# Performance work log

Measured on AMD Instinct MI355X. Metric: run time of the kernel, lower is better.

## Reference

```python
import jax, jax.numpy as jnp
import numpy as np

KH, KW, PAD, G = 3, 3, 1, 4  # kernel, padding, deformable groups


def _bilinear_gather(xg, py, px):
    """xg: [B,G,C,Hin,Win]; py,px: [B,G,K,H,W] sample coords.
    Returns [B,G,C,K,H,W] with zero padding outside the image (mmcv semantics)."""
    B, Gd, C, Hin, Win = xg.shape
    y0 = jnp.floor(py)
    x0 = jnp.floor(px)
    wy1 = py - y0
    wx1 = px - x0
    wy0 = 1.0 - wy1
    wx0 = 1.0 - wx1
    xf = xg.reshape(B, Gd, C, Hin * Win)

    def gather(yi, xi):
        valid = (yi >= 0) & (yi < Hin) & (xi >= 0) & (xi < Win)
        yc = jnp.clip(yi, 0, Hin - 1).astype(jnp.int32)
        xc = jnp.clip(xi, 0, Win - 1).astype(jnp.int32)
        lin = (yc * Win + xc).reshape(B, Gd, 1, -1)  # [B,G,1,K*H*W]
        v = jnp.take_along_axis(xf, lin, axis=3).reshape(B, Gd, C, *yi.shape[2:])
        return v * valid[:, :, None].astype(xg.dtype)

    return (gather(y0, x0) * (wy0 * wx0)[:, :, None]
            + gather(y0, x0 + 1) * (wy0 * wx1)[:, :, None]
            + gather(y0 + 1, x0) * (wy1 * wx0)[:, :, None]
            + gather(y0 + 1, x0 + 1) * (wy1 * wx1)[:, :, None])


def setup_inputs() -> dict:
    key = jax.random.key(0)
    k1, k2, k3, k4 = jax.random.split(key, 4)
    B, Cin, Cout, H, W = 8, 256, 256, 64, 64
    x = jax.random.normal(k1, (B, Cin, H, W), dtype=jnp.float32)
    shape = jax.random.normal(k2, (B, 4, H, W), dtype=jnp.float32)
    # conv_offset: 1x1 conv, 4 -> G*2*KH*KW = 72 channels, no bias
    w_offset = jax.random.normal(k3, (G * 2 * KH * KW, 4), dtype=jnp.float32) * 0.1
    # conv_adaption: deform conv weight, no bias
    w_deform = jax.random.normal(k4, (Cout, Cin, KH, KW), dtype=jnp.float32) * 0.01
    return {"x": x, "shape": shape, "w_offset": w_offset, "w_deform": w_deform}


def reference(x, shape, w_offset, w_deform):
    B, Cin, H, W = x.shape
    Cout = w_deform.shape[0]
    K = KH * KW
    # 1x1 offset-predicting conv on detached shape
    shape = jax.lax.stop_gradient(shape)
    offset = jnp.einsum('oc,bchw->bohw', w_offset, shape)  # [B, G*2*K, H, W]
    off = offset.reshape(B, G, K, 2, H, W)  # mmcv layout: (dy, dx) per tap
    dy, dx = off[:, :, :, 0], off[:, :, :, 1]  # [B,G,K,H,W]
    # base sampling grid for each kernel tap
    ky, kx = jnp.meshgrid(jnp.arange(KH), jnp.arange(KW), indexing='ij')
    ky = ky.reshape(-1)
    kx = kx.reshape(-1)
    base_y = (ky - PAD)[:, None, None] + jnp.arange(H)[None, :, None]  # [K,H,1]
    base_x = (kx - PAD)[:, None, None] + jnp.arange(W)[None, None, :]  # [K,1,W]
    py = base_y[None, None].astype(x.dtype) + dy  # [B,G,K,H,W]
    px = base_x[None, None].astype(x.dtype) + dx
    xg = x.reshape(B, G, Cin // G, H, W)
    sampled = _bilinear_gather(xg, py, px)  # [B,G,Cpg,K,H,W]
    wr = w_deform.reshape(Cout, G, Cin // G, K)
    out = jnp.einsum('ogck,bgckhw->bohw', wr, sampled)
    return jax.nn.relu(out)
```

## Files before the change

kernel.cpp:

```cpp
#include <hip/hip_runtime.h>
#include <hip/hip_bf16.h>


#define Bn   8
#define CIN  256
#define COUT 256
#define Hn   64
#define Wn   64
#define Gn   4
#define Kn   9
#define CPG  64
#define GK   36

typedef __bf16 bf16x8 __attribute__((ext_vector_type(8)));
typedef float  f32x4  __attribute__((ext_vector_type(4)));

#define SWPAD 1156
__global__ void fa_prep(const float* __restrict__ x, const float* __restrict__ w,
                        __bf16* __restrict__ xt, __bf16* __restrict__ wfrag) {
    const int bid = blockIdx.x, t = threadIdx.x;
    __shared__ __bf16 sw[16 * SWPAD];
    if (bid < 4096) {
        const int c8q = bid & 7, hwt = (bid >> 3) & 63, b = bid >> 9;
        const int hw = hwt * 64 + (t & 63);
        const int c8 = c8q * 4 + (t >> 6);
        const float* xp = x + ((size_t)(b * CIN + c8 * 8) << 12) + hw;
        bf16x8 v;
#pragma unroll
        for (int j = 0; j < 8; j++) v[j] = (__bf16)xp[(size_t)j << 12];
        *(bf16x8*)&xt[(((size_t)b << 12) + hw) * 256 + c8 * 8] = v;
    } else {
        const int mt = (bid - 4096) >> 1, gh = (bid - 4096) & 1;
        const int o0 = mt * 16, g0 = gh * 2;
        const int r = t >> 4, tr = t & 15;
        const float* wp = w + (size_t)(o0 + r) * (CIN * Kn) + g0 * (CPG * Kn);
#pragma unroll
        for (int it = 0; it < 18; it++) {
            int off = it * 64 + tr * 4;
            float4 v = *(const float4*)(wp + off);
            __bf16* d = &sw[r * SWPAD + off];
            d[0] = (__bf16)v.x; d[1] = (__bf16)v.y;
            d[2] = (__bf16)v.z; d[3] = (__bf16)v.w;
        }
        __syncthreads();
#pragma unroll
        for (int it = 0; it < 9; it++) {
            int chunk = it * 256 + t;
            int lane = chunk & 63, ks = (chunk >> 6) & 1, gkl = chunk >> 7;
            int gl = gkl / Kn, k = gkl - gl * Kn;
            int gk = g0 * Kn + gkl;
            int ol = lane & 15;
            int cbase = ks * 32 + (lane >> 4) * 8;
            bf16x8 v;
#pragma unroll
            for (int j = 0; j < 8; j++)
                v[j] = sw[ol * SWPAD + (gl * CPG + cbase + j) * Kn + k];
            *(bf16x8*)&wfrag[(((size_t)gk * 16 + mt) * 2 + ks) * 512 + lane * 8] = v;
        }
    }
}

__global__ __launch_bounds__(256, 2)
void fa_main(const __bf16* __restrict__ xt, const float* __restrict__ shp,
             const float* __restrict__ w_off, const __bf16* __restrict__ wfrag,
             float* __restrict__ out) {
    const int blk = blockIdx.x;
    const int bp = blk >> 7, h = (blk >> 1) & 63, wh = blk & 1;
    const int w0 = wh * 32;
    const int t = threadIdx.x;
    const int wid = t >> 6, lane = t & 63;
    const int col = lane & 15, quad = lane >> 4;
    const int cg = t & 7, nl0 = t >> 3;

    __shared__ int   s_iyx[GK * 64];
    __shared__ float s_fy[GK * 64];
    __shared__ float s_fx[GK * 64];
    __shared__ __align__(16) __bf16 sB[2][64 * 64];

    for (int i = t; i < GK * 64; i += 256) {
        int gk = i >> 6, n = i & 63;
        int bb = n >> 5, w = w0 + (n & 31);
        int b = bp * 2 + bb;
        int g = gk / Kn, k = gk - g * Kn;
        int ky = k / 3, kx = k - ky * 3;
        int oy = (g * Kn + k) * 2;
        float dy = 0.f, dx = 0.f;
#pragma unroll
        for (int c = 0; c < 4; c++) {
            float sv = shp[((b * 4 + c) * Hn + h) * Wn + w];
            dy = fmaf(w_off[(oy    ) * 4 + c], sv, dy);
            dx = fmaf(w_off[(oy + 1) * 4 + c], sv, dx);
        }
        float py = (float)(h + ky - 1) + dy;
        float px = (float)(w + kx - 1) + dx;
        float y0 = floorf(py), x0 = floorf(px);
        s_fy[i] = py - y0;
        s_fx[i] = px - x0;
        s_iyx[i] = (((int)y0 & 0xffff) << 16) | ((int)x0 & 0xffff);
    }

    bf16x8 c4[2][4];
    float  w4[2][4];

    auto issue = [&](int gk) {
#pragma unroll
        for (int s = 0; s < 2; s++) {
            int n = nl0 + s * 32;
            int b = bp * 2 + (n >> 5);
            int m = gk * 64 + n;
            int g = gk / Kn;
            int pk = s_iyx[m];
            int iy = pk >> 16, ix = (pk << 16) >> 16;
            float fy = s_fy[m], fx = s_fx[m];
            bool y0v = (unsigned)iy       < (unsigned)Hn;
            bool y1v = (unsigned)(iy + 1) < (unsigned)Hn;
            bool x0v = (unsigned)ix       < (unsigned)Wn;
            bool x1v = (unsigned)(ix + 1) < (unsigned)Wn;
            int yc0 = min(max(iy, 0), Hn - 1), yc1 = min(max(iy + 1, 0), Hn - 1);
            int xc0 = min(max(ix, 0), Wn - 1), xc1 = min(max(ix + 1, 0), Wn - 1);
            const __bf16* base = xt + (((size_t)b << 12)) * 256 + g * CPG + cg * 8;
            c4[s][0] = *(const bf16x8*)(base + ((size_t)(yc0 * 64 + xc0)) * 256);
            c4[s][1] = *(const bf16x8*)(base + ((size_t)(yc0 * 64 + xc1)) * 256);
            c4[s][2] = *(const bf16x8*)(base + ((size_t)(yc1 * 64 + xc0)) * 256);
            c4[s][3] = *(const bf16x8*)(base + ((size_t)(yc1 * 64 + xc1)) * 256);
            float wy1 = fy, wy0 = 1.f - fy, wx1 = fx, wx0 = 1.f - fx;
            w4[s][0] = (y0v && x0v) ? wy0 * wx0 : 0.f;
            w4[s][1] = (y0v && x1v) ? wy0 * wx1 : 0.f;
            w4[s][2] = (y1v && x0v) ? wy1 * wx0 : 0.f;
            w4[s][3] = (y1v && x1v) ? wy1 * wx1 : 0.f;
        }
    };
    auto commit = [&](int buf) {
#pragma unroll
        for (int s = 0; s < 2; s++) {
            int n = nl0 + s * 32;
            bf16x8 r;
#pragma unroll
            for (int j = 0; j < 8; j++) {
                float v = w4[s][0] * (float)c4[s][0][j] + w4[s][1] * (float)c4[s][1][j]
                        + w4[s][2] * (float)c4[s][2][j] + w4[s][3] * (float)c4[s][3][j];
                r[j] = (__bf16)v;
            }
            *(bf16x8*)&sB[buf][(n * 8 + (cg ^ (n & 7))) * 8] = r;
        }
    };
    auto loadA = [&](int gk, bf16x8 af[2][4]) {
        const __bf16* wbase = wfrag + (((size_t)gk * 16 + wid * 4) * 2) * 512;
#pragma unroll
        for (int ks = 0; ks < 2; ks++)
#pragma unroll
            for (int mt = 0; mt < 4; mt++)
                af[ks][mt] = *(const bf16x8*)(wbase + ((size_t)(mt * 2 + ks) * 64 + lane) * 8);
    };

    f32x4 acc[4][4];
#pragma unroll
    for (int mt = 0; mt < 4; mt++)
#pragma unroll
        for (int nt = 0; nt < 4; nt++) acc[mt][nt] = (f32x4){0.f, 0.f, 0.f, 0.f};

    auto domfma = [&](bf16x8 af[2][4], int buf) {
#pragma unroll
        for (int ks = 0; ks < 2; ks++) {
            bf16x8 bfv[4];
#pragma unroll
            for (int nt = 0; nt < 4; nt++) {
                int n = nt * 16 + col;
                int cq8 = ks * 4 + quad;
                bfv[nt] = *(const bf16x8*)&sB[buf][(n * 8 + (cq8 ^ (n & 7))) * 8];
            }
#pragma unroll
            for (int mt = 0; mt < 4; mt++)
#pragma unroll
                for (int nt = 0; nt < 4; nt++)
                    acc[mt][nt] = __builtin_amdgcn_mfma_f32_16x16x32_bf16(
                        af[ks][mt], bfv[nt], acc[mt][nt], 0, 0, 0);
        }
    };

    bf16x8 afA[2][4], afB[2][4];

    __syncthreads();

    loadA(0, afA);
    issue(0);
    commit(0);
    issue(1);
    __syncthreads();

    for (int gk = 0; gk < GK; gk += 2) {
        loadA(gk + 1, afB);
        commit(1);
        if (gk + 2 < GK) issue(gk + 2);
        domfma(afA, 0);
        __syncthreads();
        if (gk + 2 < GK) loadA(gk + 2, afA);
        if (gk + 2 < GK) commit(0);
        if (gk + 3 < GK) issue(gk + 3);
        domfma(afB, 1);
        __syncthreads();
    }

#pragma unroll
    for (int mt = 0; mt < 4; mt++)
#pragma unroll
        for (int r = 0; r < 4; r++) {
            int o = wid * 64 + mt * 16 + quad * 4 + r;
#pragma unroll
            for (int nt = 0; nt < 4; nt++) {
                int n = nt * 16 + col;
                int b = bp * 2 + (n >> 5);
                int w = w0 + (n & 31);
                out[(((size_t)(b * COUT + o)) << 12) + h * Wn + w] =
                    fmaxf(acc[mt][nt][r], 0.f);
            }
        }
}

extern "C" void kernel_launch(void* const* d_in, const int* in_sizes, int n_in,
                              void* d_out, int out_size, void* d_ws, size_t ws_size,
                              hipStream_t stream) {
    const float* x     = (const float*)d_in[0];
    const float* shp   = (const float*)d_in[1];
    const float* w_off = (const float*)d_in[2];
    const float* w_def = (const float*)d_in[3];
    float* out = (float*)d_out;
    __bf16* wfrag = (__bf16*)d_ws;
    __bf16* xt    = (__bf16*)((char*)d_ws + (2u << 20));

    fa_prep<<<4096 + 32, 256, 0, stream>>>(x, w_def, xt, wfrag);
    fa_main<<<512, 256, 0, stream>>>(xt, shp, w_off, wfrag, out);
}
```

Before: 154.3 us.

## Use 512-thread blocks with eight waves splitting output channels in main kernel

```diff
diff --git a/kernel.cpp b/kernel.cpp
--- a/kernel.cpp
+++ b/kernel.cpp
@@ -60,7 +60,7 @@
     }
 }
 
-__global__ __launch_bounds__(256, 2)
+__global__ __launch_bounds__(512, 4)
 void fa_main(const __bf16* __restrict__ xt, const float* __restrict__ shp,
              const float* __restrict__ w_off, const __bf16* __restrict__ wfrag,
              float* __restrict__ out) {
@@ -70,14 +70,14 @@
     const int t = threadIdx.x;
     const int wid = t >> 6, lane = t & 63;
     const int col = lane & 15, quad = lane >> 4;
-    const int cg = t & 7, nl0 = t >> 3;
+    const int cg = t & 7, nl = (t >> 3) & 63;
 
     __shared__ int   s_iyx[GK * 64];
     __shared__ float s_fy[GK * 64];
     __shared__ float s_fx[GK * 64];
     __shared__ __align__(16) __bf16 sB[2][64 * 64];
 
-    for (int i = t; i < GK * 64; i += 256) {
+    for (int i = t; i < GK * 64; i += 512) {
         int gk = i >> 6, n = i & 63;
         int bb = n >> 5, w = w0 + (n & 31);
         int b = bp * 2 + bb;
@@ -99,67 +99,68 @@
         s_iyx[i] = (((int)y0 & 0xffff) << 16) | ((int)x0 & 0xffff);
     }
 
-    bf16x8 c4[2][4];
-    float  w4[2][4];
+    bf16x8 c4[4];
+    float  w4[4];
 
     auto issue = [&](int gk) {
-#pragma unroll
-        for (int s = 0; s < 2; s++) {
-            int n = nl0 + s * 32;
-            int b = bp * 2 + (n >> 5);
-            int m = gk * 64 + n;
-            int g = gk / Kn;
-            int pk = s_iyx[m];
-            int iy = pk >> 16, ix = (pk << 16) >> 16;
-            float fy = s_fy[m], fx = s_fx[m];
-            bool y0v = (unsigned)iy       < (unsigned)Hn;
-            bool y1v = (unsigned)(iy + 1) < (unsigned)Hn;
-            bool x0v = (unsigned)ix       < (unsigned)Wn;
-            bool x1v = (unsigned)(ix + 1) < (unsigned)Wn;
-            int yc0 = min(max(iy, 0), Hn - 1), yc1 = min(max(iy + 1, 0), Hn - 1);
-            int xc0 = min(max(ix, 0), Wn - 1), xc1 = min(max(ix + 1, 0), Wn - 1);
-            const __bf16* base = xt + (((size_t)b << 12)) * 256 + g * CPG + cg * 8;
-            c4[s][0] = *(const bf16x8*)(base + ((size_t)(yc0 * 64 + xc0)) * 256);
-            c4[s][1] = *(const bf16x8*)(base + ((size_t)(yc0 * 64 + xc1)) * 256);
-            c4[s][2] = *(const bf16x8*)(base + ((size_t)(yc1 * 64 + xc0)) * 256);
-            c4[s][3] = *(const bf16x8*)(base + ((size_t)(yc1 * 64 + xc1)) * 256);
-            float wy1 = fy, wy0 = 1.f - fy, wx1 = fx, wx0 = 1.f - fx;
-            w4[s][0] = (y0v && x0v) ? wy0 * wx0 : 0.f;
-            w4[s][1] = (y0v && x1v) ? wy0 * wx1 : 0.f;
-            w4[s][2] = (y1v && x0v) ? wy1 * wx0 : 0.f;
-            w4[s][3] = (y1v && x1v) ? wy1 * wx1 : 0.f;
-        }
+        int b = bp * 2 + (nl >> 5);
+        int m = gk * 64 + nl;
+        int g = gk / Kn;
+        int pk = s_iyx[m];
+        int iy = pk >> 16, ix = (pk << 16) >> 16;
+        float fy = s_fy[m], fx = s_fx[m];
+        bool y0v = (unsigned)iy       < (unsigned)Hn;
+        bool y1v = (unsigned)(iy + 1) < (unsigned)Hn;
+        bool x0v = (unsigned)ix       < (unsigned)Wn;
+        bool x1v = (unsigned)(ix + 1) < (unsigned)Wn;
+        int yc0 = min(max(iy, 0), Hn - 1), yc1 = min(max(iy + 1, 0), Hn - 1);
+        int xc0 = min(max(ix, 0), Wn - 1), xc1 = min(max(ix + 1, 0), Wn - 1);
+        const __bf16* base = xt + (((size_t)b << 12)) * 256 + g * CPG + cg * 8;
+        c4[0] = *(const bf16x8*)(base + ((size_t)(yc0 * 64 + xc0)) * 256);
+        c4[1] = *(const bf16x8*)(base + ((size_t)(yc0 * 64 + xc1)) * 256);
+        c4[2] = *(const bf16x8*)(base + ((size_t)(yc1 * 64 + xc0)) * 256);
+        c4[3] = *(const bf16x8*)(base + ((size_t)(yc1 * 64 + xc1)) * 256);
+        float wy1 = fy, wy0 = 1.f - fy, wx1 = fx, wx0 = 1.f - fx;
+        w4[0] = (y0v && x0v) ? wy0 * wx0 : 0.f;
+        w4[1] = (y0v && x1v) ? wy0 * wx1 : 0.f;
+        w4[2] = (y1v && x0v) ? wy1 * wx0 : 0.f;
+        w4[3] = (y1v && x1v) ? wy1 * wx1 : 0.f;
     };
     auto commit = [&](int buf) {
-#pragma unroll
-        for (int s = 0; s < 2; s++) {
-            int n = nl0 + s * 32;
-            bf16x8 r;
-#pragma unroll
-            for (int j = 0; j < 8; j++) {
-                float v = w4[s][0] * (float)c4[s][0][j] + w4[s][1] * (float)c4[s][1][j]
-                        + w4[s][2] * (float)c4[s][2][j] + w4[s][3] * (float)c4[s][3][j];
-                r[j] = (__bf16)v;
-            }
-            *(bf16x8*)&sB[buf][(n * 8 + (cg ^ (n & 7))) * 8] = r;
-        }
+        bf16x8 r;
+#pragma unroll
+        for (int j = 0; j < 8; j++) {
+            float v = w4[0] * (float)c4[0][j] + w4[1] * (float)c4[1][j]
+                    + w4[2] * (float)c4[2][j] + w4[3] * (float)c4[3][j];
+            r[j] = (__bf16)v;
+        }
+        *(bf16x8*)&sB[buf][(nl * 8 + (cg ^ (nl & 7))) * 8] = r;
     };
-    auto loadA = [&](int gk, bf16x8 af[2][4]) {
-        const __bf16* wbase = wfrag + (((size_t)gk * 16 + wid * 4) * 2) * 512;
+
+    f32x4 acc[2][4];
+#pragma unroll
+    for (int mt = 0; mt < 2; mt++)
+#pragma unroll
+        for (int nt = 0; nt < 4; nt++) acc[mt][nt] = (f32x4){0.f, 0.f, 0.f, 0.f};
+
+    __syncthreads();
+
+    issue(0);
+    commit(0);
+    issue(1);
+    __syncthreads();
+
+    for (int gk = 0; gk < GK; gk++) {
+        const int buf = gk & 1;
+        const __bf16* wbase = wfrag + (((size_t)gk * 16 + wid * 2) * 2) * 512;
+        bf16x8 af[2][2];
 #pragma unroll
         for (int ks = 0; ks < 2; ks++)
 #pragma unroll
-            for (int mt = 0; mt < 4; mt++)
+            for (int mt = 0; mt < 2; mt++)
                 af[ks][mt] = *(const bf16x8*)(wbase + ((size_t)(mt * 2 + ks) * 64 + lane) * 8);
-    };
-
-    f32x4 acc[4][4];
-#pragma unroll
-    for (int mt = 0; mt < 4; mt++)
-#pragma unroll
-        for (int nt = 0; nt < 4; nt++) acc[mt][nt] = (f32x4){0.f, 0.f, 0.f, 0.f};
-
-    auto domfma = [&](bf16x8 af[2][4], int buf) {
+        if (gk + 1 < GK) commit(buf ^ 1);
+        if (gk + 2 < GK) issue(gk + 2);
 #pragma unroll
         for (int ks = 0; ks < 2; ks++) {
             bf16x8 bfv[4];
@@ -170,42 +171,20 @@
                 bfv[nt] = *(const bf16x8*)&sB[buf][(n * 8 + (cq8 ^ (n & 7))) * 8];
             }
 #pragma unroll
-            for (int mt = 0; mt < 4; mt++)
+            for (int mt = 0; mt < 2; mt++)
 #pragma unroll
                 for (int nt = 0; nt < 4; nt++)
                     acc[mt][nt] = __builtin_amdgcn_mfma_f32_16x16x32_bf16(
                         af[ks][mt], bfv[nt], acc[mt][nt], 0, 0, 0);
         }
-    };
-
-    bf16x8 afA[2][4], afB[2][4];
-
-    __syncthreads();
-
-    loadA(0, afA);
-    issue(0);
-    commit(0);
-    issue(1);
-    __syncthreads();
-
-    for (int gk = 0; gk < GK; gk += 2) {
-        loadA(gk + 1, afB);
-        commit(1);
-        if (gk + 2 < GK) issue(gk + 2);
-        domfma(afA, 0);
-        __syncthreads();
-        if (gk + 2 < GK) loadA(gk + 2, afA);
-        if (gk + 2 < GK) commit(0);
-        if (gk + 3 < GK) issue(gk + 3);
-        domfma(afB, 1);
         __syncthreads();
     }
 
 #pragma unroll
-    for (int mt = 0; mt < 4; mt++)
+    for (int mt = 0; mt < 2; mt++)
 #pragma unroll
         for (int r = 0; r < 4; r++) {
-            int o = wid * 64 + mt * 16 + quad * 4 + r;
+            int o = wid * 32 + mt * 16 + quad * 4 + r;
 #pragma unroll
             for (int nt = 0; nt < 4; nt++) {
                 int n = nt * 16 + col;
@@ -229,5 +208,5 @@
     __bf16* xt    = (__bf16*)((char*)d_ws + (2u << 20));
 
     fa_prep<<<4096 + 32, 256, 0, stream>>>(x, w_def, xt, wfrag);
-    fa_main<<<512, 256, 0, stream>>>(xt, shp, w_off, wfrag, out);
+    fa_main<<<512, 512, 0, stream>>>(xt, shp, w_off, wfrag, out);
 }
```

Result: faster. 147.4 us (-4.5%).
